# Kernel optimization log

Measured on AMD Instinct MI355X. Metric: run time of the kernel, lower is better.

The kernel has to match this reference:

```python
import jax, jax.numpy as jnp
import numpy as np

E = 8            # num_experts
H = 1024         # hidden_size
I = 1024         # moe_intermediate_dim
T = 8192         # total tokens (sum of per-expert counts; no padding, grouped_mm path)
# Imbalanced routing, sums exactly to T
COUNTS = np.array([512, 1536, 1024, 768, 1280, 896, 1152, 1024], dtype=np.int32)


def setup_inputs() -> dict:
    key = jax.random.key(0)
    k_x, k_gu, k_d = jax.random.split(key, 3)
    x = jax.random.normal(k_x, (T, H), dtype=jnp.float32)
    # Weights stored pre-transposed: (E, H, 2I) and (E, I, H)
    gate_up_proj = jax.random.normal(k_gu, (E, H, 2 * I), dtype=jnp.float32) * (1.0 / np.sqrt(H))
    down_proj = jax.random.normal(k_d, (E, I, H), dtype=jnp.float32) * (1.0 / np.sqrt(I))
    num_tokens_per_expert = jnp.asarray(COUNTS)  # int32, sums to T
    return {
        "x": x,
        "gate_up_proj": gate_up_proj,
        "down_proj": down_proj,
        "num_tokens_per_expert": num_tokens_per_expert,
    }


def reference(x, gate_up_proj, down_proj, num_tokens_per_expert):
    # Grouped GEMM 1: [T,H] x [E,H,2I] with ragged group sizes -> [T,2I]
    gate_up = jax.lax.ragged_dot(x, gate_up_proj, group_sizes=num_tokens_per_expert)
    gate, up = jnp.split(gate_up, 2, axis=-1)
    h = jax.nn.silu(gate) * up  # SwiGLU: silu(gate) * up, [T,I]
    # Grouped GEMM 2: [T,I] x [E,I,H] -> [T,H]
    out = jax.lax.ragged_dot(h, down_proj, group_sizes=num_tokens_per_expert)
    return out.astype(x.dtype)
```

## Files before the change

kernel.cpp:

```cpp
#include <hip/hip_runtime.h>
#include <hip/hip_bf16.h>
#include <stdint.h>

#define E_ 8
#define H_ 1024
#define I_ 1024
#define T_ 8192
#define BM 128
#define BK 32
#define NKT 32

typedef __attribute__((ext_vector_type(4))) float f32x4;
typedef __attribute__((ext_vector_type(8))) short bf16x8;
typedef __attribute__((ext_vector_type(8))) unsigned short u16x8;

__device__ __forceinline__ unsigned short f2bf(float f) {
  union { float f; unsigned int u; } v; v.f = f;
  unsigned int lsb = (v.u >> 16) & 1u;
  v.u += 0x7fffu + lsb;
  return (unsigned short)(v.u >> 16);
}

__device__ __forceinline__ void gload_lds16(const void* g, void* l) {
  __builtin_amdgcn_global_load_lds(
      (const __attribute__((address_space(1))) unsigned int*)g,
      (__attribute__((address_space(3))) unsigned int*)l,
      16, 0, 0);
}

__device__ __forceinline__ void find_tile(const int* counts, int ty,
                                          int& row_start, int& rows, int& expert) {
  int tacc = 0, off = 0;
  expert = 0; row_start = 0; rows = BM;
  #pragma unroll
  for (int e = 0; e < E_; ++e) {
    int c = counts[e];
    int te = (c + BM - 1) >> 7;
    if (ty >= tacc && ty < tacc + te) {
      expert = e;
      int lt = ty - tacc;
      row_start = off + lt * BM;
      rows = min(BM, c - lt * BM);
    }
    tacc += te; off += c;
  }
}

__global__ __launch_bounds__(256) void convert_x(
    const float* __restrict__ x, unsigned short* __restrict__ xb) {
  int id = blockIdx.x;
  #pragma unroll
  for (int it = 0; it < 4; ++it) {
    int i = id * 4096 + it * 1024 + threadIdx.x * 4;
    float4 v = *reinterpret_cast<const float4*>(x + i);
    ushort4 o;
    o.x = f2bf(v.x); o.y = f2bf(v.y); o.z = f2bf(v.z); o.w = f2bf(v.w);
    *reinterpret_cast<ushort4*>(xb + i) = o;
  }
}

__device__ __forceinline__ void transpose_role(const float* __restrict__ inp,
                                               unsigned short* __restrict__ outp,
                                               int R, int C, int bx, int by,
                                               float* tile ) {
  int c0 = bx * 64, r0 = by * 128;
  int lc = threadIdx.x & 15;
  int lrw = threadIdx.x >> 4;
  #pragma unroll
  for (int p = 0; p < 8; ++p) {
    int r = p * 16 + lrw;
    float4 v = *reinterpret_cast<const float4*>(
        inp + (size_t)(r0 + r) * C + c0 + lc * 4);
    float* t = &tile[r * 65 + lc * 4];
    t[0] = v.x; t[1] = v.y; t[2] = v.z; t[3] = v.w;
  }
  __syncthreads();
  int lq = threadIdx.x & 15;
  int co = threadIdx.x >> 4;
  #pragma unroll
  for (int p = 0; p < 4; ++p) {
    int cc = p * 16 + co;
    u16x8 o;
    #pragma unroll
    for (int i = 0; i < 8; ++i)
      o[i] = f2bf(tile[(8 * lq + i) * 65 + cc]);
    *reinterpret_cast<u16x8*>(&outp[(size_t)(c0 + cc) * R + r0 + 8 * lq]) = o;
  }
}

__global__ __launch_bounds__(256) void transpose_w(
    const float* __restrict__ w1, unsigned short* __restrict__ w1t,
    const float* __restrict__ w2, unsigned short* __restrict__ w2t) {
  __shared__ float tile[128 * 65];
  int id = blockIdx.x;
  if (id < 2048) {
    int bx = id & 31, by = (id >> 5) & 7, bz = id >> 8;
    transpose_role(w1 + (size_t)bz * H_ * 2 * I_,
                   w1t + (size_t)bz * H_ * 2 * I_, H_, 2 * I_, bx, by, tile);
    return;
  }
  int tb = id - 2048;
  int bx = tb & 15, by = (tb >> 4) & 7, bz = tb >> 7;
  transpose_role(w2 + (size_t)bz * I_ * H_,
                 w2t + (size_t)bz * I_ * H_, I_, H_, bx, by, tile);
}

#define GLDS (BM * BK + 256 * BK)
__global__ __launch_bounds__(256, 2) void gemm1_swiglu(
    const unsigned short* __restrict__ X,
    const unsigned short* __restrict__ W1T,
    const int* __restrict__ counts,
    unsigned short* __restrict__ Hout) {
  __shared__ unsigned short pool[3 * GLDS];
  int id = blockIdx.x;
  int swz = (id & 7) * 64 + (id >> 3);
  int bn = swz & 7;
  int tyid = swz >> 3;
  int row_start, rows, expert;
  find_tile(counts, tyid, row_start, rows, expert);
  int tid = threadIdx.x, wid = tid >> 6, lane = tid & 63;
  const unsigned short* Wp = W1T + (size_t)expert * (2 * I_) * H_;

  f32x4 acc[8][4];
  #pragma unroll
  for (int m = 0; m < 8; ++m)
    #pragma unroll
    for (int n = 0; n < 4; ++n) acc[m][n] = {0.f, 0.f, 0.f, 0.f};

  int l4 = lane >> 2;
  int csw = ((lane & 3) ^ ((l4 >> 1) & 3)) * 8;
  int lr = lane & 15;
  int ck = ((lane >> 4) ^ ((lr >> 1) & 3)) * 8;

#define STAGE1(buf, kt) do {                                                   \
    int k0 = (kt) * BK + csw;                                                  \
    unsigned short* Ab = pool + (buf) * GLDS;                                  \
    unsigned short* Bb = Ab + BM * BK;                                         \
    _Pragma("unroll")                                                          \
    for (int i = 0; i < 2; ++i) {                                              \
      int r = wid * 32 + i * 16;                                               \
      int gr = row_start + min(r + l4, rows - 1);                              \
      gload_lds16(X + (size_t)gr * H_ + k0, Ab + r * BK);                      \
    }                                                                          \
    _Pragma("unroll")                                                          \
    for (int i = 0; i < 4; ++i) {                                              \
      int r = wid * 64 + i * 16;                                               \
      int rb = r + l4;                                                         \
      int sub = rb & 63, ow = rb >> 6;                                         \
      int col = (sub < 32) ? (bn * 128 + ow * 32 + sub)                        \
                           : (I_ + bn * 128 + ow * 32 + sub - 32);             \
      gload_lds16(Wp + (size_t)col * H_ + k0, Bb + r * BK);                    \
    }                                                                          \
  } while (0)

  STAGE1(0, 0);
  STAGE1(1, 1);
  for (int kt = 0; kt < NKT; ++kt) {
    STAGE1((kt + 2) % 3, min(kt + 2, NKT - 1));
    asm volatile("s_waitcnt vmcnt(12)" ::: "memory");
    __builtin_amdgcn_sched_barrier(0);
    __builtin_amdgcn_s_barrier();
    const unsigned short* Ab = pool + (kt % 3) * GLDS;
    const unsigned short* Bb = Ab + BM * BK;
    bf16x8 a[8], b[4];
    #pragma unroll
    for (int m = 0; m < 8; ++m)
      a[m] = *reinterpret_cast<const bf16x8*>(&Ab[(m * 16 + lr) * BK + ck]);
    #pragma unroll
    for (int n = 0; n < 4; ++n)
      b[n] = *reinterpret_cast<const bf16x8*>(&Bb[(wid * 64 + n * 16 + lr) * BK + ck]);
    __builtin_amdgcn_s_setprio(1);
    #pragma unroll
    for (int m = 0; m < 8; ++m)
      #pragma unroll
      for (int n = 0; n < 4; ++n)
        acc[m][n] = __builtin_amdgcn_mfma_f32_16x16x32_bf16(a[m], b[n], acc[m][n], 0, 0, 0);
    __builtin_amdgcn_s_setprio(0);
    __builtin_amdgcn_s_barrier();
  }
#undef STAGE1

  int lq = lane >> 4;
  #pragma unroll
  for (int m = 0; m < 8; ++m)
    #pragma unroll
    for (int n = 0; n < 2; ++n) {
      f32x4 g = acc[m][n], u = acc[m][n + 2];
      #pragma unroll
      for (int r = 0; r < 4; ++r) {
        int rl = m * 16 + lq * 4 + r;
        if (rl < rows) {
          float gv = g[r];
          float hv = (gv / (1.f + __expf(-gv))) * u[r];
          Hout[(size_t)(row_start + rl) * I_ + bn * 128 + wid * 32 + n * 16 + lr] = f2bf(hv);
        }
      }
    }
}

__global__ __launch_bounds__(256, 2) void gemm2(
    const unsigned short* __restrict__ Hin,
    const unsigned short* __restrict__ W2T,
    const int* __restrict__ counts,
    float* __restrict__ Out) {
  __shared__ unsigned short pool[3 * GLDS];
  int id = blockIdx.x;
  int swz = (id & 7) * 32 + (id >> 3);
  int bn = swz & 3;
  int tyid = swz >> 2;
  int row_start, rows, expert;
  find_tile(counts, tyid, row_start, rows, expert);
  int tid = threadIdx.x, wid = tid >> 6, lane = tid & 63;
  const unsigned short* Wp = W2T + (size_t)expert * H_ * I_;

  f32x4 acc[8][4];
  #pragma unroll
  for (int m = 0; m < 8; ++m)
    #pragma unroll
    for (int n = 0; n < 4; ++n) acc[m][n] = {0.f, 0.f, 0.f, 0.f};

  int l4 = lane >> 2;
  int csw = ((lane & 3) ^ ((l4 >> 1) & 3)) * 8;
  int lr = lane & 15;
  int ck = ((lane >> 4) ^ ((lr >> 1) & 3)) * 8;

#define STAGE2(buf, kt) do {                                                   \
    int k0 = (kt) * BK + csw;                                                  \
    unsigned short* Ab = pool + (buf) * GLDS;                                  \
    unsigned short* Bb = Ab + BM * BK;                                         \
    _Pragma("unroll")                                                          \
    for (int i = 0; i < 2; ++i) {                                              \
      int r = wid * 32 + i * 16;                                               \
      int gr = row_start + min(r + l4, rows - 1);                              \
      gload_lds16(Hin + (size_t)gr * I_ + k0, Ab + r * BK);                    \
    }                                                                          \
    _Pragma("unroll")                                                          \
    for (int i = 0; i < 4; ++i) {                                              \
      int r = wid * 64 + i * 16;                                               \
      int col = bn * 256 + r + l4;                                             \
      gload_lds16(Wp + (size_t)col * I_ + k0, Bb + r * BK);                    \
    }                                                                          \
  } while (0)

  STAGE2(0, 0);
  STAGE2(1, 1);
  for (int kt = 0; kt < NKT; ++kt) {
    STAGE2((kt + 2) % 3, min(kt + 2, NKT - 1));
    asm volatile("s_waitcnt vmcnt(12)" ::: "memory");
    __builtin_amdgcn_sched_barrier(0);
    __builtin_amdgcn_s_barrier();
    const unsigned short* Ab = pool + (kt % 3) * GLDS;
    const unsigned short* Bb = Ab + BM * BK;
    bf16x8 a[8], b[4];
    #pragma unroll
    for (int m = 0; m < 8; ++m)
      a[m] = *reinterpret_cast<const bf16x8*>(&Ab[(m * 16 + lr) * BK + ck]);
    #pragma unroll
    for (int n = 0; n < 4; ++n)
      b[n] = *reinterpret_cast<const bf16x8*>(&Bb[(wid * 64 + n * 16 + lr) * BK + ck]);
    __builtin_amdgcn_s_setprio(1);
    #pragma unroll
    for (int m = 0; m < 8; ++m)
      #pragma unroll
      for (int n = 0; n < 4; ++n)
        acc[m][n] = __builtin_amdgcn_mfma_f32_16x16x32_bf16(a[m], b[n], acc[m][n], 0, 0, 0);
    __builtin_amdgcn_s_setprio(0);
    __builtin_amdgcn_s_barrier();
  }
#undef STAGE2

  int lq = lane >> 4;
  #pragma unroll
  for (int m = 0; m < 8; ++m)
    #pragma unroll
    for (int n = 0; n < 4; ++n)
      #pragma unroll
      for (int r = 0; r < 4; ++r) {
        int rl = m * 16 + lq * 4 + r;
        if (rl < rows)
          Out[(size_t)(row_start + rl) * H_ + bn * 256 + wid * 64 + n * 16 + lr] =
              acc[m][n][r];
      }
}

extern "C" void kernel_launch(void* const* d_in, const int* in_sizes, int n_in,
                              void* d_out, int out_size, void* d_ws, size_t ws_size,
                              hipStream_t stream) {
  const float* x  = (const float*)d_in[0];
  const float* w1 = (const float*)d_in[1];
  const float* w2 = (const float*)d_in[2];
  const int* counts = (const int*)d_in[3];
  float* out = (float*)d_out;

  char* ws = (char*)d_ws;
  unsigned short* xb  = (unsigned short*)ws;
  unsigned short* w1t = (unsigned short*)(ws + (size_t)T_ * H_ * 2);
  unsigned short* w2t = (unsigned short*)(ws + (size_t)T_ * H_ * 2
                                             + (size_t)E_ * 2 * I_ * H_ * 2);
  unsigned short* hbuf = (unsigned short*)(ws + (size_t)T_ * H_ * 2
                                              + (size_t)E_ * 2 * I_ * H_ * 2
                                              + (size_t)E_ * H_ * I_ * 2);

  convert_x<<<2048, 256, 0, stream>>>(x, xb);
  transpose_w<<<3072, 256, 0, stream>>>(w1, w1t, w2, w2t);
  gemm1_swiglu<<<512, 256, 0, stream>>>(xb, w1t, counts, hbuf);
  gemm2<<<256, 256, 0, stream>>>(hbuf, w2t, counts, out);
}
```

Measured before the change: 102.9 us.

## Restructure grouped GEMMs to 8-wave blocks with BK=64 and interleaved prefetch

Both grouped GEMM kernels now launch 512 threads (8 waves in a 2x4 grid) instead of 256, each wave owning a 64x64 sub-tile. The K step doubles to 64 with a new XOR swizzle for LDS. Global-to-LDS prefetches for the next stage are spread across four MFMA phases separated by barriers instead of issued in one burst. The aim is to overlap memory traffic with MFMA work and to cut the accumulator registers per wave, at the cost of more barriers and one block per CU.

```diff
diff --git a/kernel.cpp b/kernel.cpp
--- a/kernel.cpp
+++ b/kernel.cpp
@@ -7,8 +7,6 @@
 #define I_ 1024
 #define T_ 8192
 #define BM 128
-#define BK 32
-#define NKT 32
 
 typedef __attribute__((ext_vector_type(4))) float f32x4;
 typedef __attribute__((ext_vector_type(8))) short bf16x8;
@@ -105,180 +103,275 @@
                  w2t + (size_t)bz * I_ * H_, I_, H_, bx, by, tile);
 }
 
-#define GLDS (BM * BK + 256 * BK)
-__global__ __launch_bounds__(256, 2) void gemm1_swiglu(
+#define GBUF 24576
+#define GNKT 16
+
+__device__ __forceinline__ bf16x8 ldfrag(const unsigned short* b, int row, int ck) {
+  return *reinterpret_cast<const bf16x8*>(&b[row * 64 + ck]);
+}
+
+__global__ __launch_bounds__(512, 1) void gemm1_swiglu(
     const unsigned short* __restrict__ X,
     const unsigned short* __restrict__ W1T,
     const int* __restrict__ counts,
     unsigned short* __restrict__ Hout) {
-  __shared__ unsigned short pool[3 * GLDS];
+  __shared__ unsigned short pool[3 * GBUF];
   int id = blockIdx.x;
   int swz = (id & 7) * 64 + (id >> 3);
   int bn = swz & 7;
   int tyid = swz >> 3;
   int row_start, rows, expert;
   find_tile(counts, tyid, row_start, rows, expert);
-  int tid = threadIdx.x, wid = tid >> 6, lane = tid & 63;
+  int tid = threadIdx.x, w = tid >> 6, lane = tid & 63;
+  int wr = w >> 2, wc = w & 3;
   const unsigned short* Wp = W1T + (size_t)expert * (2 * I_) * H_;
 
-  f32x4 acc[8][4];
-  #pragma unroll
-  for (int m = 0; m < 8; ++m)
+  f32x4 acc[4][4];
+  #pragma unroll
+  for (int m = 0; m < 4; ++m)
     #pragma unroll
     for (int n = 0; n < 4; ++n) acc[m][n] = {0.f, 0.f, 0.f, 0.f};
 
-  int l4 = lane >> 2;
-  int csw = ((lane & 3) ^ ((l4 >> 1) & 3)) * 8;
-  int lr = lane & 15;
-  int ck = ((lane >> 4) ^ ((lr >> 1) & 3)) * 8;
-
-#define STAGE1(buf, kt) do {                                                   \
-    int k0 = (kt) * BK + csw;                                                  \
-    unsigned short* Ab = pool + (buf) * GLDS;                                  \
-    unsigned short* Bb = Ab + BM * BK;                                         \
-    _Pragma("unroll")                                                          \
-    for (int i = 0; i < 2; ++i) {                                              \
-      int r = wid * 32 + i * 16;                                               \
-      int gr = row_start + min(r + l4, rows - 1);                              \
-      gload_lds16(X + (size_t)gr * H_ + k0, Ab + r * BK);                      \
-    }                                                                          \
-    _Pragma("unroll")                                                          \
-    for (int i = 0; i < 4; ++i) {                                              \
-      int r = wid * 64 + i * 16;                                               \
-      int rb = r + l4;                                                         \
-      int sub = rb & 63, ow = rb >> 6;                                         \
-      int col = (sub < 32) ? (bn * 128 + ow * 32 + sub)                        \
-                           : (I_ + bn * 128 + ow * 32 + sub - 32);             \
-      gload_lds16(Wp + (size_t)col * H_ + k0, Bb + r * BK);                    \
-    }                                                                          \
+  int lr = lane & 15, hi = lane >> 4;
+  int ck0 = (hi ^ (lr & 7)) * 8;
+  int ck1 = ((4 + hi) ^ (lr & 7)) * 8;
+  int sr = lane >> 3;
+  int cgo = ((lane & 7) ^ sr) * 8;
+
+#define S1A(buf, kt, i) do {                                                   \
+    int r = (w * 2 + (i)) * 8 + sr;                                            \
+    int gr = row_start + min(r, rows - 1);                                     \
+    gload_lds16(X + (size_t)gr * H_ + (kt) * 64 + cgo,                         \
+                pool + (buf) * GBUF + (w * 2 + (i)) * 512);                    \
   } while (0)
-
-  STAGE1(0, 0);
-  STAGE1(1, 1);
-  for (int kt = 0; kt < NKT; ++kt) {
-    STAGE1((kt + 2) % 3, min(kt + 2, NKT - 1));
-    asm volatile("s_waitcnt vmcnt(12)" ::: "memory");
+#define S1B(buf, kt, i) do {                                                   \
+    int rb = (w * 4 + (i)) * 8 + sr;                                           \
+    int wcv = rb >> 6, sub = rb & 63;                                          \
+    int col = (sub < 32) ? (bn * 128 + wcv * 32 + sub)                         \
+                         : (I_ + bn * 128 + wcv * 32 + (sub - 32));            \
+    gload_lds16(Wp + (size_t)col * H_ + (kt) * 64 + cgo,                       \
+                pool + (buf) * GBUF + 8192 + (w * 4 + (i)) * 512);             \
+  } while (0)
+
+  S1A(0, 0, 0); S1A(0, 0, 1); S1B(0, 0, 0); S1B(0, 0, 1); S1B(0, 0, 2); S1B(0, 0, 3);
+  S1A(1, 1, 0); S1A(1, 1, 1); S1B(1, 1, 0); S1B(1, 1, 1); S1B(1, 1, 2); S1B(1, 1, 3);
+  asm volatile("s_waitcnt vmcnt(6)" ::: "memory");
+  __builtin_amdgcn_sched_barrier(0);
+  __builtin_amdgcn_s_barrier();
+
+  for (int t = 0; t < GNKT; ++t) {
+    const unsigned short* Ab = pool + (t % 3) * GBUF;
+    const unsigned short* Bb = Ab + 8192;
+    int dst = (t + 2) % 3;
+    int nk = t + 2;
+    bool pre = (nk < GNKT);
+    bf16x8 bf[4], af[2];
+    #pragma unroll
+    for (int n = 0; n < 4; ++n) bf[n] = ldfrag(Bb, wc * 64 + n * 16 + lr, ck0);
+    af[0] = ldfrag(Ab, wr * 64 + lr, ck0);
+    af[1] = ldfrag(Ab, wr * 64 + 16 + lr, ck0);
+    if (pre) S1A(dst, nk, 0);
+    __builtin_amdgcn_s_barrier();
+    __builtin_amdgcn_s_setprio(1);
+    #pragma unroll
+    for (int m = 0; m < 2; ++m)
+      #pragma unroll
+      for (int n = 0; n < 4; ++n)
+        acc[m][n] = __builtin_amdgcn_mfma_f32_16x16x32_bf16(af[m], bf[n], acc[m][n], 0, 0, 0);
+    __builtin_amdgcn_s_setprio(0);
+    __builtin_amdgcn_s_barrier();
+    af[0] = ldfrag(Ab, wr * 64 + 32 + lr, ck0);
+    af[1] = ldfrag(Ab, wr * 64 + 48 + lr, ck0);
+    if (pre) S1A(dst, nk, 1);
+    __builtin_amdgcn_s_barrier();
+    __builtin_amdgcn_s_setprio(1);
+    #pragma unroll
+    for (int m = 0; m < 2; ++m)
+      #pragma unroll
+      for (int n = 0; n < 4; ++n)
+        acc[m + 2][n] = __builtin_amdgcn_mfma_f32_16x16x32_bf16(af[m], bf[n], acc[m + 2][n], 0, 0, 0);
+    __builtin_amdgcn_s_setprio(0);
+    __builtin_amdgcn_s_barrier();
+    #pragma unroll
+    for (int n = 0; n < 4; ++n) bf[n] = ldfrag(Bb, wc * 64 + n * 16 + lr, ck1);
+    af[0] = ldfrag(Ab, wr * 64 + lr, ck1);
+    af[1] = ldfrag(Ab, wr * 64 + 16 + lr, ck1);
+    if (pre) { S1B(dst, nk, 0); S1B(dst, nk, 1); }
+    __builtin_amdgcn_s_barrier();
+    __builtin_amdgcn_s_setprio(1);
+    #pragma unroll
+    for (int m = 0; m < 2; ++m)
+      #pragma unroll
+      for (int n = 0; n < 4; ++n)
+        acc[m][n] = __builtin_amdgcn_mfma_f32_16x16x32_bf16(af[m], bf[n], acc[m][n], 0, 0, 0);
+    __builtin_amdgcn_s_setprio(0);
+    __builtin_amdgcn_s_barrier();
+    af[0] = ldfrag(Ab, wr * 64 + 32 + lr, ck1);
+    af[1] = ldfrag(Ab, wr * 64 + 48 + lr, ck1);
+    if (pre) {
+      S1B(dst, nk, 2); S1B(dst, nk, 3);
+      asm volatile("s_waitcnt vmcnt(6)" ::: "memory");
+    } else {
+      asm volatile("s_waitcnt vmcnt(0)" ::: "memory");
+    }
     __builtin_amdgcn_sched_barrier(0);
     __builtin_amdgcn_s_barrier();
-    const unsigned short* Ab = pool + (kt % 3) * GLDS;
-    const unsigned short* Bb = Ab + BM * BK;
-    bf16x8 a[8], b[4];
-    #pragma unroll
-    for (int m = 0; m < 8; ++m)
-      a[m] = *reinterpret_cast<const bf16x8*>(&Ab[(m * 16 + lr) * BK + ck]);
-    #pragma unroll
-    for (int n = 0; n < 4; ++n)
-      b[n] = *reinterpret_cast<const bf16x8*>(&Bb[(wid * 64 + n * 16 + lr) * BK + ck]);
-    __builtin_amdgcn_s_setprio(1);
-    #pragma unroll
-    for (int m = 0; m < 8; ++m)
-      #pragma unroll
-      for (int n = 0; n < 4; ++n)
-        acc[m][n] = __builtin_amdgcn_mfma_f32_16x16x32_bf16(a[m], b[n], acc[m][n], 0, 0, 0);
-    __builtin_amdgcn_s_setprio(0);
-    __builtin_amdgcn_s_barrier();
-  }
-#undef STAGE1
+    __builtin_amdgcn_s_setprio(1);
+    #pragma unroll
+    for (int m = 0; m < 2; ++m)
+      #pragma unroll
+      for (int n = 0; n < 4; ++n)
+        acc[m + 2][n] = __builtin_amdgcn_mfma_f32_16x16x32_bf16(af[m], bf[n], acc[m + 2][n], 0, 0, 0);
+    __builtin_amdgcn_s_setprio(0);
+    __builtin_amdgcn_s_barrier();
+  }
+#undef S1A
+#undef S1B
 
   int lq = lane >> 4;
   #pragma unroll
-  for (int m = 0; m < 8; ++m)
+  for (int m = 0; m < 4; ++m)
     #pragma unroll
     for (int n = 0; n < 2; ++n) {
       f32x4 g = acc[m][n], u = acc[m][n + 2];
       #pragma unroll
       for (int r = 0; r < 4; ++r) {
-        int rl = m * 16 + lq * 4 + r;
+        int rl = wr * 64 + m * 16 + lq * 4 + r;
         if (rl < rows) {
           float gv = g[r];
           float hv = (gv / (1.f + __expf(-gv))) * u[r];
-          Hout[(size_t)(row_start + rl) * I_ + bn * 128 + wid * 32 + n * 16 + lr] = f2bf(hv);
+          Hout[(size_t)(row_start + rl) * I_ + bn * 128 + wc * 32 + n * 16 + lr] = f2bf(hv);
         }
       }
     }
 }
 
-__global__ __launch_bounds__(256, 2) void gemm2(
+__global__ __launch_bounds__(512, 1) void gemm2(
     const unsigned short* __restrict__ Hin,
     const unsigned short* __restrict__ W2T,
     const int* __restrict__ counts,
     float* __restrict__ Out) {
-  __shared__ unsigned short pool[3 * GLDS];
+  __shared__ unsigned short pool[3 * GBUF];
   int id = blockIdx.x;
   int swz = (id & 7) * 32 + (id >> 3);
   int bn = swz & 3;
   int tyid = swz >> 2;
   int row_start, rows, expert;
   find_tile(counts, tyid, row_start, rows, expert);
-  int tid = threadIdx.x, wid = tid >> 6, lane = tid & 63;
+  int tid = threadIdx.x, w = tid >> 6, lane = tid & 63;
+  int wr = w >> 2, wc = w & 3;
   const unsigned short* Wp = W2T + (size_t)expert * H_ * I_;
 
-  f32x4 acc[8][4];
-  #pragma unroll
-  for (int m = 0; m < 8; ++m)
+  f32x4 acc[4][4];
+  #pragma unroll
+  for (int m = 0; m < 4; ++m)
     #pragma unroll
     for (int n = 0; n < 4; ++n) acc[m][n] = {0.f, 0.f, 0.f, 0.f};
 
-  int l4 = lane >> 2;
-  int csw = ((lane & 3) ^ ((l4 >> 1) & 3)) * 8;
-  int lr = lane & 15;
-  int ck = ((lane >> 4) ^ ((lr >> 1) & 3)) * 8;
-
-#define STAGE2(buf, kt) do {                                                   \
-    int k0 = (kt) * BK + csw;                                                  \
-    unsigned short* Ab = pool + (buf) * GLDS;                                  \
-    unsigned short* Bb = Ab + BM * BK;                                         \
-    _Pragma("unroll")                                                          \
-    for (int i = 0; i < 2; ++i) {                                              \
-      int r = wid * 32 + i * 16;                                               \
-      int gr = row_start + min(r + l4, rows - 1);                              \
-      gload_lds16(Hin + (size_t)gr * I_ + k0, Ab + r * BK);                    \
-    }                                                                          \
-    _Pragma("unroll")                                                          \
-    for (int i = 0; i < 4; ++i) {                                              \
-      int r = wid * 64 + i * 16;                                               \
-      int col = bn * 256 + r + l4;                                             \
-      gload_lds16(Wp + (size_t)col * I_ + k0, Bb + r * BK);                    \
-    }                                                                          \
+  int lr = lane & 15, hi = lane >> 4;
+  int ck0 = (hi ^ (lr & 7)) * 8;
+  int ck1 = ((4 + hi) ^ (lr & 7)) * 8;
+  int sr = lane >> 3;
+  int cgo = ((lane & 7) ^ sr) * 8;
+
+#define S2A(buf, kt, i) do {                                                   \
+    int r = (w * 2 + (i)) * 8 + sr;                                            \
+    int gr = row_start + min(r, rows - 1);                                     \
+    gload_lds16(Hin + (size_t)gr * I_ + (kt) * 64 + cgo,                       \
+                pool + (buf) * GBUF + (w * 2 + (i)) * 512);                    \
   } while (0)
-
-  STAGE2(0, 0);
-  STAGE2(1, 1);
-  for (int kt = 0; kt < NKT; ++kt) {
-    STAGE2((kt + 2) % 3, min(kt + 2, NKT - 1));
-    asm volatile("s_waitcnt vmcnt(12)" ::: "memory");
+#define S2B(buf, kt, i) do {                                                   \
+    int rb = (w * 4 + (i)) * 8 + sr;                                           \
+    int col = bn * 256 + rb;                                                   \
+    gload_lds16(Wp + (size_t)col * I_ + (kt) * 64 + cgo,                       \
+                pool + (buf) * GBUF + 8192 + (w * 4 + (i)) * 512);             \
+  } while (0)
+
+  S2A(0, 0, 0); S2A(0, 0, 1); S2B(0, 0, 0); S2B(0, 0, 1); S2B(0, 0, 2); S2B(0, 0, 3);
+  S2A(1, 1, 0); S2A(1, 1, 1); S2B(1, 1, 0); S2B(1, 1, 1); S2B(1, 1, 2); S2B(1, 1, 3);
+  asm volatile("s_waitcnt vmcnt(6)" ::: "memory");
+  __builtin_amdgcn_sched_barrier(0);
+  __builtin_amdgcn_s_barrier();
+
+  for (int t = 0; t < GNKT; ++t) {
+    const unsigned short* Ab = pool + (t % 3) * GBUF;
+    const unsigned short* Bb = Ab + 8192;
+    int dst = (t + 2) % 3;
+    int nk = t + 2;
+    bool pre = (nk < GNKT);
+    bf16x8 bf[4], af[2];
+    #pragma unroll
+    for (int n = 0; n < 4; ++n) bf[n] = ldfrag(Bb, wc * 64 + n * 16 + lr, ck0);
+    af[0] = ldfrag(Ab, wr * 64 + lr, ck0);
+    af[1] = ldfrag(Ab, wr * 64 + 16 + lr, ck0);
+    if (pre) S2A(dst, nk, 0);
+    __builtin_amdgcn_s_barrier();
+    __builtin_amdgcn_s_setprio(1);
+    #pragma unroll
+    for (int m = 0; m < 2; ++m)
+      #pragma unroll
+      for (int n = 0; n < 4; ++n)
+        acc[m][n] = __builtin_amdgcn_mfma_f32_16x16x32_bf16(af[m], bf[n], acc[m][n], 0, 0, 0);
+    __builtin_amdgcn_s_setprio(0);
+    __builtin_amdgcn_s_barrier();
+    af[0] = ldfrag(Ab, wr * 64 + 32 + lr, ck0);
+    af[1] = ldfrag(Ab, wr * 64 + 48 + lr, ck0);
+    if (pre) S2A(dst, nk, 1);
+    __builtin_amdgcn_s_barrier();
+    __builtin_amdgcn_s_setprio(1);
+    #pragma unroll
+    for (int m = 0; m < 2; ++m)
+      #pragma unroll
+      for (int n = 0; n < 4; ++n)
+        acc[m + 2][n] = __builtin_amdgcn_mfma_f32_16x16x32_bf16(af[m], bf[n], acc[m + 2][n], 0, 0, 0);
+    __builtin_amdgcn_s_setprio(0);
+    __builtin_amdgcn_s_barrier();
+    #pragma unroll
+    for (int n = 0; n < 4; ++n) bf[n] = ldfrag(Bb, wc * 64 + n * 16 + lr, ck1);
+    af[0] = ldfrag(Ab, wr * 64 + lr, ck1);
+    af[1] = ldfrag(Ab, wr * 64 + 16 + lr, ck1);
+    if (pre) { S2B(dst, nk, 0); S2B(dst, nk, 1); }
+    __builtin_amdgcn_s_barrier();
+    __builtin_amdgcn_s_setprio(1);
+    #pragma unroll
+    for (int m = 0; m < 2; ++m)
+      #pragma unroll
+      for (int n = 0; n < 4; ++n)
+        acc[m][n] = __builtin_amdgcn_mfma_f32_16x16x32_bf16(af[m], bf[n], acc[m][n], 0, 0, 0);
+    __builtin_amdgcn_s_setprio(0);
+    __builtin_amdgcn_s_barrier();
+    af[0] = ldfrag(Ab, wr * 64 + 32 + lr, ck1);
+    af[1] = ldfrag(Ab, wr * 64 + 48 + lr, ck1);
+    if (pre) {
+      S2B(dst, nk, 2); S2B(dst, nk, 3);
+      asm volatile("s_waitcnt vmcnt(6)" ::: "memory");
+    } else {
+      asm volatile("s_waitcnt vmcnt(0)" ::: "memory");
+    }
     __builtin_amdgcn_sched_barrier(0);
     __builtin_amdgcn_s_barrier();
-    const unsigned short* Ab = pool + (kt % 3) * GLDS;
-    const unsigned short* Bb = Ab + BM * BK;
-    bf16x8 a[8], b[4];
-    #pragma unroll
-    for (int m = 0; m < 8; ++m)
-      a[m] = *reinterpret_cast<const bf16x8*>(&Ab[(m * 16 + lr) * BK + ck]);
+    __builtin_amdgcn_s_setprio(1);
+    #pragma unroll
+    for (int m = 0; m < 2; ++m)
+      #pragma unroll
+      for (int n = 0; n < 4; ++n)
+        acc[m + 2][n] = __builtin_amdgcn_mfma_f32_16x16x32_bf16(af[m], bf[n], acc[m + 2][n], 0, 0, 0);
+    __builtin_amdgcn_s_setprio(0);
+    __builtin_amdgcn_s_barrier();
+  }
+#undef S2A
+#undef S2B
+
+  int lq = lane >> 4;
+  #pragma unroll
+  for (int m = 0; m < 4; ++m)
     #pragma unroll
     for (int n = 0; n < 4; ++n)
-      b[n] = *reinterpret_cast<const bf16x8*>(&Bb[(wid * 64 + n * 16 + lr) * BK + ck]);
-    __builtin_amdgcn_s_setprio(1);
-    #pragma unroll
-    for (int m = 0; m < 8; ++m)
-      #pragma unroll
-      for (int n = 0; n < 4; ++n)
-        acc[m][n] = __builtin_amdgcn_mfma_f32_16x16x32_bf16(a[m], b[n], acc[m][n], 0, 0, 0);
-    __builtin_amdgcn_s_setprio(0);
-    __builtin_amdgcn_s_barrier();
-  }
-#undef STAGE2
-
-  int lq = lane >> 4;
-  #pragma unroll
-  for (int m = 0; m < 8; ++m)
-    #pragma unroll
-    for (int n = 0; n < 4; ++n)
       #pragma unroll
       for (int r = 0; r < 4; ++r) {
-        int rl = m * 16 + lq * 4 + r;
+        int rl = wr * 64 + m * 16 + lq * 4 + r;
         if (rl < rows)
-          Out[(size_t)(row_start + rl) * H_ + bn * 256 + wid * 64 + n * 16 + lr] =
+          Out[(size_t)(row_start + rl) * H_ + bn * 256 + wc * 64 + n * 16 + lr] =
               acc[m][n][r];
       }
 }
@@ -303,6 +396,6 @@
 
   convert_x<<<2048, 256, 0, stream>>>(x, xb);
   transpose_w<<<3072, 256, 0, stream>>>(w1, w1t, w2, w2t);
-  gemm1_swiglu<<<512, 256, 0, stream>>>(xb, w1t, counts, hbuf);
-  gemm2<<<256, 256, 0, stream>>>(hbuf, w2t, counts, out);
-}
+  gemm1_swiglu<<<512, 512, 0, stream>>>(xb, w1t, counts, hbuf);
+  gemm2<<<256, 512, 0, stream>>>(hbuf, w2t, counts, out);
+}
```

Result: no change. 101.8 us (-1.0%).

## Fuse preprocessing kernels and restructure gemm2 into 8-wave interleaved pipeline

Applied to the files above, without the earlier changes.

Merges the x conversion and weight transpose kernels into one launch, removing a launch and the gap between them. Rewrites gemm2 to use 512 threads (8 waves in a 2x4 grid), BK=64 with an XOR-swizzled LDS layout, and a triple-buffered pipeline whose global-to-LDS loads are split into chunks interleaved with the MFMA phases. The goal is better latency hiding and fewer registers per wave, at the cost of more barriers per k-step and one block per CU.

```diff
diff --git a/kernel.cpp b/kernel.cpp
--- a/kernel.cpp
+++ b/kernel.cpp
@@ -46,19 +46,6 @@
   }
 }
 
-__global__ __launch_bounds__(256) void convert_x(
-    const float* __restrict__ x, unsigned short* __restrict__ xb) {
-  int id = blockIdx.x;
-  #pragma unroll
-  for (int it = 0; it < 4; ++it) {
-    int i = id * 4096 + it * 1024 + threadIdx.x * 4;
-    float4 v = *reinterpret_cast<const float4*>(x + i);
-    ushort4 o;
-    o.x = f2bf(v.x); o.y = f2bf(v.y); o.z = f2bf(v.z); o.w = f2bf(v.w);
-    *reinterpret_cast<ushort4*>(xb + i) = o;
-  }
-}
-
 __device__ __forceinline__ void transpose_role(const float* __restrict__ inp,
                                                unsigned short* __restrict__ outp,
                                                int R, int C, int bx, int by,
@@ -88,18 +75,31 @@
   }
 }
 
-__global__ __launch_bounds__(256) void transpose_w(
+__global__ __launch_bounds__(256) void preproc_all(
+    const float* __restrict__ x, unsigned short* __restrict__ xb,
     const float* __restrict__ w1, unsigned short* __restrict__ w1t,
     const float* __restrict__ w2, unsigned short* __restrict__ w2t) {
   __shared__ float tile[128 * 65];
   int id = blockIdx.x;
   if (id < 2048) {
-    int bx = id & 31, by = (id >> 5) & 7, bz = id >> 8;
+    #pragma unroll
+    for (int it = 0; it < 4; ++it) {
+      int i = id * 4096 + it * 1024 + threadIdx.x * 4;
+      float4 v = *reinterpret_cast<const float4*>(x + i);
+      ushort4 o;
+      o.x = f2bf(v.x); o.y = f2bf(v.y); o.z = f2bf(v.z); o.w = f2bf(v.w);
+      *reinterpret_cast<ushort4*>(xb + i) = o;
+    }
+    return;
+  }
+  if (id < 4096) {
+    int tb = id - 2048;
+    int bx = tb & 31, by = (tb >> 5) & 7, bz = tb >> 8;
     transpose_role(w1 + (size_t)bz * H_ * 2 * I_,
                    w1t + (size_t)bz * H_ * 2 * I_, H_, 2 * I_, bx, by, tile);
     return;
   }
-  int tb = id - 2048;
+  int tb = id - 4096;
   int bx = tb & 15, by = (tb >> 4) & 7, bz = tb >> 7;
   transpose_role(w2 + (size_t)bz * I_ * H_,
                  w2t + (size_t)bz * I_ * H_, I_, H_, bx, by, tile);
@@ -198,87 +198,139 @@
     }
 }
 
-__global__ __launch_bounds__(256, 2) void gemm2(
+#define GBUF 24576
+#define GNKT 16
+
+__device__ __forceinline__ bf16x8 ldfrag(const unsigned short* b, int row, int ck) {
+  return *reinterpret_cast<const bf16x8*>(&b[row * 64 + ck]);
+}
+
+__global__ __launch_bounds__(512, 1) void gemm2(
     const unsigned short* __restrict__ Hin,
     const unsigned short* __restrict__ W2T,
     const int* __restrict__ counts,
     float* __restrict__ Out) {
-  __shared__ unsigned short pool[3 * GLDS];
+  __shared__ unsigned short pool[3 * GBUF];
   int id = blockIdx.x;
   int swz = (id & 7) * 32 + (id >> 3);
   int bn = swz & 3;
   int tyid = swz >> 2;
   int row_start, rows, expert;
   find_tile(counts, tyid, row_start, rows, expert);
-  int tid = threadIdx.x, wid = tid >> 6, lane = tid & 63;
+  int tid = threadIdx.x, w = tid >> 6, lane = tid & 63;
+  int wr = w >> 2, wc = w & 3;
   const unsigned short* Wp = W2T + (size_t)expert * H_ * I_;
 
-  f32x4 acc[8][4];
-  #pragma unroll
-  for (int m = 0; m < 8; ++m)
+  f32x4 acc[4][4];
+  #pragma unroll
+  for (int m = 0; m < 4; ++m)
     #pragma unroll
     for (int n = 0; n < 4; ++n) acc[m][n] = {0.f, 0.f, 0.f, 0.f};
 
-  int l4 = lane >> 2;
-  int csw = ((lane & 3) ^ ((l4 >> 1) & 3)) * 8;
-  int lr = lane & 15;
-  int ck = ((lane >> 4) ^ ((lr >> 1) & 3)) * 8;
-
-#define STAGE2(buf, kt) do {                                                   \
-    int k0 = (kt) * BK + csw;                                                  \
-    unsigned short* Ab = pool + (buf) * GLDS;                                  \
-    unsigned short* Bb = Ab + BM * BK;                                         \
-    _Pragma("unroll")                                                          \
-    for (int i = 0; i < 2; ++i) {                                              \
-      int r = wid * 32 + i * 16;                                               \
-      int gr = row_start + min(r + l4, rows - 1);                              \
-      gload_lds16(Hin + (size_t)gr * I_ + k0, Ab + r * BK);                    \
-    }                                                                          \
-    _Pragma("unroll")                                                          \
-    for (int i = 0; i < 4; ++i) {                                              \
-      int r = wid * 64 + i * 16;                                               \
-      int col = bn * 256 + r + l4;                                             \
-      gload_lds16(Wp + (size_t)col * I_ + k0, Bb + r * BK);                    \
-    }                                                                          \
+  int lr = lane & 15, hi = lane >> 4;
+  int ck0 = (hi ^ (lr & 7)) * 8;
+  int ck1 = ((4 + hi) ^ (lr & 7)) * 8;
+  int sr = lane >> 3;
+  int cgo = ((lane & 7) ^ sr) * 8;
+
+#define S2A(buf, kt, i) do {                                                   \
+    int r = (w * 2 + (i)) * 8 + sr;                                            \
+    int gr = row_start + min(r, rows - 1);                                     \
+    gload_lds16(Hin + (size_t)gr * I_ + (kt) * 64 + cgo,                       \
+                pool + (buf) * GBUF + (w * 2 + (i)) * 512);                    \
   } while (0)
-
-  STAGE2(0, 0);
-  STAGE2(1, 1);
-  for (int kt = 0; kt < NKT; ++kt) {
-    STAGE2((kt + 2) % 3, min(kt + 2, NKT - 1));
-    asm volatile("s_waitcnt vmcnt(12)" ::: "memory");
+#define S2B(buf, kt, i) do {                                                   \
+    int rb = (w * 4 + (i)) * 8 + sr;                                           \
+    int col = bn * 256 + rb;                                                   \
+    gload_lds16(Wp + (size_t)col * I_ + (kt) * 64 + cgo,                       \
+                pool + (buf) * GBUF + 8192 + (w * 4 + (i)) * 512);             \
+  } while (0)
+
+  S2A(0, 0, 0); S2A(0, 0, 1); S2B(0, 0, 0); S2B(0, 0, 1); S2B(0, 0, 2); S2B(0, 0, 3);
+  S2A(1, 1, 0); S2A(1, 1, 1); S2B(1, 1, 0); S2B(1, 1, 1); S2B(1, 1, 2); S2B(1, 1, 3);
+  asm volatile("s_waitcnt vmcnt(6)" ::: "memory");
+  __builtin_amdgcn_sched_barrier(0);
+  __builtin_amdgcn_s_barrier();
+
+  for (int t = 0; t < GNKT; ++t) {
+    const unsigned short* Ab = pool + (t % 3) * GBUF;
+    const unsigned short* Bb = Ab + 8192;
+    int dst = (t + 2) % 3;
+    int nk = t + 2;
+    bool pre = (nk < GNKT);
+    bf16x8 bf[4], af[2];
+    #pragma unroll
+    for (int n = 0; n < 4; ++n) bf[n] = ldfrag(Bb, wc * 64 + n * 16 + lr, ck0);
+    af[0] = ldfrag(Ab, wr * 64 + lr, ck0);
+    af[1] = ldfrag(Ab, wr * 64 + 16 + lr, ck0);
+    if (pre) S2A(dst, nk, 0);
+    __builtin_amdgcn_s_barrier();
+    __builtin_amdgcn_s_setprio(1);
+    #pragma unroll
+    for (int m = 0; m < 2; ++m)
+      #pragma unroll
+      for (int n = 0; n < 4; ++n)
+        acc[m][n] = __builtin_amdgcn_mfma_f32_16x16x32_bf16(af[m], bf[n], acc[m][n], 0, 0, 0);
+    __builtin_amdgcn_s_setprio(0);
+    __builtin_amdgcn_s_barrier();
+    af[0] = ldfrag(Ab, wr * 64 + 32 + lr, ck0);
+    af[1] = ldfrag(Ab, wr * 64 + 48 + lr, ck0);
+    if (pre) S2A(dst, nk, 1);
+    __builtin_amdgcn_s_barrier();
+    __builtin_amdgcn_s_setprio(1);
+    #pragma unroll
+    for (int m = 0; m < 2; ++m)
+      #pragma unroll
+      for (int n = 0; n < 4; ++n)
+        acc[m + 2][n] = __builtin_amdgcn_mfma_f32_16x16x32_bf16(af[m], bf[n], acc[m + 2][n], 0, 0, 0);
+    __builtin_amdgcn_s_setprio(0);
+    __builtin_amdgcn_s_barrier();
+    #pragma unroll
+    for (int n = 0; n < 4; ++n) bf[n] = ldfrag(Bb, wc * 64 + n * 16 + lr, ck1);
+    af[0] = ldfrag(Ab, wr * 64 + lr, ck1);
+    af[1] = ldfrag(Ab, wr * 64 + 16 + lr, ck1);
+    if (pre) { S2B(dst, nk, 0); S2B(dst, nk, 1); }
+    __builtin_amdgcn_s_barrier();
+    __builtin_amdgcn_s_setprio(1);
+    #pragma unroll
+    for (int m = 0; m < 2; ++m)
+      #pragma unroll
+      for (int n = 0; n < 4; ++n)
+        acc[m][n] = __builtin_amdgcn_mfma_f32_16x16x32_bf16(af[m], bf[n], acc[m][n], 0, 0, 0);
+    __builtin_amdgcn_s_setprio(0);
+    __builtin_amdgcn_s_barrier();
+    af[0] = ldfrag(Ab, wr * 64 + 32 + lr, ck1);
+    af[1] = ldfrag(Ab, wr * 64 + 48 + lr, ck1);
+    if (pre) {
+      S2B(dst, nk, 2); S2B(dst, nk, 3);
+      asm volatile("s_waitcnt vmcnt(6)" ::: "memory");
+    } else {
+      asm volatile("s_waitcnt vmcnt(0)" ::: "memory");
+    }
     __builtin_amdgcn_sched_barrier(0);
     __builtin_amdgcn_s_barrier();
-    const unsigned short* Ab = pool + (kt % 3) * GLDS;
-    const unsigned short* Bb = Ab + BM * BK;
-    bf16x8 a[8], b[4];
-    #pragma unroll
-    for (int m = 0; m < 8; ++m)
-      a[m] = *reinterpret_cast<const bf16x8*>(&Ab[(m * 16 + lr) * BK + ck]);
+    __builtin_amdgcn_s_setprio(1);
+    #pragma unroll
+    for (int m = 0; m < 2; ++m)
+      #pragma unroll
+      for (int n = 0; n < 4; ++n)
+        acc[m + 2][n] = __builtin_amdgcn_mfma_f32_16x16x32_bf16(af[m], bf[n], acc[m + 2][n], 0, 0, 0);
+    __builtin_amdgcn_s_setprio(0);
+    __builtin_amdgcn_s_barrier();
+  }
+#undef S2A
+#undef S2B
+
+  int lq = lane >> 4;
+  #pragma unroll
+  for (int m = 0; m < 4; ++m)
     #pragma unroll
     for (int n = 0; n < 4; ++n)
-      b[n] = *reinterpret_cast<const bf16x8*>(&Bb[(wid * 64 + n * 16 + lr) * BK + ck]);
-    __builtin_amdgcn_s_setprio(1);
-    #pragma unroll
-    for (int m = 0; m < 8; ++m)
-      #pragma unroll
-      for (int n = 0; n < 4; ++n)
-        acc[m][n] = __builtin_amdgcn_mfma_f32_16x16x32_bf16(a[m], b[n], acc[m][n], 0, 0, 0);
-    __builtin_amdgcn_s_setprio(0);
-    __builtin_amdgcn_s_barrier();
-  }
-#undef STAGE2
-
-  int lq = lane >> 4;
-  #pragma unroll
-  for (int m = 0; m < 8; ++m)
-    #pragma unroll
-    for (int n = 0; n < 4; ++n)
       #pragma unroll
       for (int r = 0; r < 4; ++r) {
-        int rl = m * 16 + lq * 4 + r;
+        int rl = wr * 64 + m * 16 + lq * 4 + r;
         if (rl < rows)
-          Out[(size_t)(row_start + rl) * H_ + bn * 256 + wid * 64 + n * 16 + lr] =
+          Out[(size_t)(row_start + rl) * H_ + bn * 256 + wc * 64 + n * 16 + lr] =
               acc[m][n][r];
       }
 }
@@ -301,8 +353,7 @@
                                               + (size_t)E_ * 2 * I_ * H_ * 2
                                               + (size_t)E_ * H_ * I_ * 2);
 
-  convert_x<<<2048, 256, 0, stream>>>(x, xb);
-  transpose_w<<<3072, 256, 0, stream>>>(w1, w1t, w2, w2t);
+  preproc_all<<<5120, 256, 0, stream>>>(x, xb, w1, w1t, w2, w2t);
   gemm1_swiglu<<<512, 256, 0, stream>>>(xb, w1t, counts, hbuf);
-  gemm2<<<256, 256, 0, stream>>>(hbuf, w2t, counts, out);
-}
+  gemm2<<<256, 512, 0, stream>>>(hbuf, w2t, counts, out);
+}
```

After: 100.9 us. No clear change (-1.9%).
